# Kernel tuning notes

Measured on AMD Instinct MI355X. Metric: run time of the kernel, lower is better.

The kernel has to match this reference:

```python
import jax, jax.numpy as jnp
import numpy as np

N = 100000      # nodes
E = 1600000     # edges (avg degree 16)
F_IN = 64       # state_size
H = 128         # hidden_channels
L = 3           # nb_hidden_layers


def setup_inputs() -> dict:
    key = jax.random.key(0)
    ks = jax.random.split(key, 10)
    x = jax.random.normal(ks[0], (N, F_IN), dtype=jnp.float32)
    edge_index = jax.random.randint(ks[1], (2, E), 0, N, dtype=jnp.int32)
    # GCNConv params (glorot-ish scale), bias=True by default in PyG
    W1 = jax.random.normal(ks[2], (F_IN, H), jnp.float32) * (1.0 / np.sqrt(F_IN))
    b1 = jnp.zeros((H,), jnp.float32)
    W2 = jax.random.normal(ks[3], (L, H, H), jnp.float32) * (1.0 / np.sqrt(H))
    b2 = jnp.zeros((L, H), jnp.float32)
    W3 = jax.random.normal(ks[4], (H, 1), jnp.float32) * (1.0 / np.sqrt(H))
    b3 = jnp.zeros((1,), jnp.float32)
    return {"x": x, "edge_index": edge_index, "W1": W1, "b1": b1,
            "W2": W2, "b2": b2, "W3": W3, "b3": b3}


def _gcn_norm(edge_index):
    """Add self-loops and compute symmetric normalization (PyG GCNConv default)."""
    loop = jnp.arange(N, dtype=edge_index.dtype)
    src = jnp.concatenate([edge_index[0], loop])  # [E+N]
    dst = jnp.concatenate([edge_index[1], loop])
    deg = jax.ops.segment_sum(jnp.ones_like(dst, dtype=jnp.float32), dst, num_segments=N)
    dinv = jnp.where(deg > 0, jax.lax.rsqrt(deg), 0.0)
    norm = dinv[src] * dinv[dst]                  # [E+N]
    return src, dst, norm


def _gcn_conv(x, src, dst, norm, W, b):
    h = x @ W                                     # [N, F_out] linear first
    msg = h[src] * norm[:, None]                  # gather + scale, [E+N, F_out]
    agg = jax.ops.segment_sum(msg, dst, num_segments=N)  # scatter-add
    return agg + b


def reference(x, edge_index, W1, b1, W2, b2, W3, b3):
    src, dst, norm = _gcn_norm(edge_index)
    h = jax.nn.relu(_gcn_conv(x, src, dst, norm, W1, b1))
    for i in range(L):  # fixed small layer count
        h = jax.nn.relu(_gcn_conv(h, src, dst, norm, W2[i], b2[i]))
    out = _gcn_conv(h, src, dst, norm, W3, b3)    # [N, 1]
    return out
```

## Files before the change

kernel.cpp:

```cpp
#include <hip/hip_runtime.h>
#include <hip/hip_bf16.h>

#define DIV_UP(a,b) (((a)+(b)-1)/(b))

typedef __attribute__((ext_vector_type(8))) short short8v;
typedef __attribute__((ext_vector_type(4))) float f32x4;
typedef _Float16 half8v __attribute__((ext_vector_type(8)));

__device__ inline unsigned short f2bf(float f){
  unsigned u = __float_as_uint(f);
  u += 0x7FFFu + ((u >> 16) & 1u);
  return (unsigned short)(u >> 16);
}
__device__ inline float bf2f(unsigned short h){ return __uint_as_float(((unsigned)h) << 16); }

__global__ __launch_bounds__(256) void k_count_r(const int* __restrict__ dst, int* __restrict__ counts8,
                                                 int E, int N){
  const int g   = blockIdx.x & 7;
  const int bi  = blockIdx.x >> 3;
  const int bpg = gridDim.x >> 3;
  const int chunkE = (E + 7) >> 3;
  const int lo = g*chunkE;
  const int hi = min(lo + chunkE, E);
  int* base = counts8 + (size_t)g*N;
  for (int e = lo + bi*256 + threadIdx.x; e < hi; e += bpg*256)
    atomicAdd(&base[dst[e]], 1);
}

__global__ __launch_bounds__(256) void k_fill_g(const int* __restrict__ src, const int* __restrict__ dst,
                                                const int* __restrict__ rowptr, int* __restrict__ fill,
                                                int* __restrict__ csr, int E, int N){
  const int g   = blockIdx.x & 7;
  const int bi  = blockIdx.x >> 3;
  const int bpg = gridDim.x >> 3;
  const int chunk = (N + 7) >> 3;
  const int lo = g*chunk;
  const int hi = min(lo + chunk, N);
  for (int e = bi*256 + threadIdx.x; e < E; e += bpg*256){
    int d = dst[e];
    if (d >= lo && d < hi){
      int pos = rowptr[d] + atomicAdd(&fill[d], 1);
      csr[pos] = src[e];
    }
  }
}

__global__ __launch_bounds__(1024) void k_scan1(const int* __restrict__ counts8, int* __restrict__ rowptr,
                                                int* __restrict__ bsum, float* __restrict__ dinv, int N){
  __shared__ int s[1024];
  int t = threadIdx.x, g = blockIdx.x*1024 + t;
  int v = 0;
  if (g < N){
    #pragma unroll
    for (int j = 0; j < 8; ++j) v += counts8[(size_t)j*N + g];
    dinv[g] = rsqrtf((float)(v + 1));
  }
  s[t] = v; __syncthreads();
  for (int off = 1; off < 1024; off <<= 1){
    int u = (t >= off) ? s[t-off] : 0; __syncthreads();
    s[t] += u; __syncthreads();
  }
  if (g < N) rowptr[g] = s[t] - v;
  if (t == 1023) bsum[blockIdx.x] = s[1023];
}

__global__ __launch_bounds__(128) void k_scan2(const int* __restrict__ bsum, int* __restrict__ boff,
                                               int nb, int* __restrict__ rowptr, int N){
  __shared__ int s[128];
  int t = threadIdx.x;
  int v = (t < nb) ? bsum[t] : 0;
  s[t] = v; __syncthreads();
  for (int off = 1; off < 128; off <<= 1){
    int u = (t >= off) ? s[t-off] : 0; __syncthreads();
    s[t] += u; __syncthreads();
  }
  if (t < nb) boff[t] = s[t] - v;
  if (t == 127) rowptr[N] = s[127];
}

__global__ __launch_bounds__(1024) void k_scan3(int* __restrict__ rowptr, const int* __restrict__ boff, int N){
  int g = blockIdx.x*1024 + threadIdx.x;
  if (g < N) rowptr[g] += boff[blockIdx.x];
}

__global__ __launch_bounds__(256) void k_prep_x(const float* __restrict__ x, const float* __restrict__ dinv,
                                                _Float16* __restrict__ xs, int N){
  int idx = blockIdx.x*256 + threadIdx.x;
  if (idx >= N*8) return;
  int row = idx >> 3, c = (idx & 7) * 8;
  float d = dinv[row];
  float4 a = *(const float4*)(x + (size_t)row*64 + c);
  float4 b = *(const float4*)(x + (size_t)row*64 + c + 4);
  half8v o;
  o[0]=(_Float16)(d*a.x); o[1]=(_Float16)(d*a.y); o[2]=(_Float16)(d*a.z); o[3]=(_Float16)(d*a.w);
  o[4]=(_Float16)(d*b.x); o[5]=(_Float16)(d*b.y); o[6]=(_Float16)(d*b.z); o[7]=(_Float16)(d*b.w);
  *(half8v*)(xs + (size_t)row*64 + c) = o;
}

__global__ __launch_bounds__(256) void k_split_w(const float* __restrict__ W1, const float* __restrict__ W2,
                                                 unsigned short* __restrict__ W1h, unsigned short* __restrict__ W1l,
                                                 unsigned short* __restrict__ W2h, unsigned short* __restrict__ W2l,
                                                 int L){
  int idx = blockIdx.x*256 + threadIdx.x;
  int n1 = 64*128;
  if (idx < n1){
    int j = idx & 7, lane = (idx >> 3) & 63, t = idx >> 9;
    int kc = t >> 3, nt = t & 7;
    int tcol = lane & 15, quad = lane >> 4;
    int k = kc*32 + quad*8 + j, n = nt*16 + tcol;
    float v = W1[k*128 + n];
    unsigned short hi = f2bf(v);
    W1h[idx] = hi; W1l[idx] = f2bf(v - bf2f(hi));
  } else {
    int idx2 = idx - n1;
    if (idx2 >= L*128*128) return;
    int i = idx2 >> 14, r = idx2 & 16383;
    int j = r & 7, lane = (r >> 3) & 63, t = r >> 9;
    int kc = t >> 3, nt = t & 7;
    int tcol = lane & 15, quad = lane >> 4;
    int k = kc*32 + quad*8 + j, n = nt*16 + tcol;
    float v = W2[(size_t)i*16384 + k*128 + n];
    unsigned short hi = f2bf(v);
    W2h[idx2] = hi; W2l[idx2] = f2bf(v - bf2f(hi));
  }
}

__global__ __launch_bounds__(256) void k_layer1(const _Float16* __restrict__ xs, const int* __restrict__ rowptr,
                                                const int* __restrict__ csr, const float* __restrict__ dinv,
                                                const unsigned short* __restrict__ W1h, const unsigned short* __restrict__ W1l,
                                                const float* __restrict__ b1,
                                                const unsigned short* __restrict__ W2h0, const unsigned short* __restrict__ W2l0,
                                                _Float16* __restrict__ pout, int N){
  constexpr int XS = 72, HS = 136;
  __shared__ __align__(16) char smem[32*HS*2*2];
  unsigned short (*Xh)[XS] = (unsigned short(*)[XS])smem;
  unsigned short (*Xl)[XS] = (unsigned short(*)[XS])(smem + 32*XS*2);
  unsigned short (*Hh)[HS] = (unsigned short(*)[HS])smem;
  unsigned short (*Hl)[HS] = (unsigned short(*)[HS])(smem + 32*HS*2);

  const int tid = threadIdx.x;
  const int node0 = blockIdx.x*32;

  {
    const int nl = tid >> 3;
    const int c  = (tid & 7) * 8;
    const _Float16* xc = xs + c;
    int node = node0 + nl;
    if (node < N){
      const float dn = dinv[node];
      int e = rowptr[node], end = rowptr[node+1];
      half8v sv = *(const half8v*)(xs + (size_t)node*64 + c);
      float a[8];
      #pragma unroll
      for (int j = 0; j < 8; ++j) a[j] = (float)sv[j];
      for (; e + 4 <= end; e += 4){
        int s0 = csr[e], s1 = csr[e+1], s2 = csr[e+2], s3 = csr[e+3];
        half8v v0 = *(const half8v*)(xc + (size_t)s0*64);
        half8v v1 = *(const half8v*)(xc + (size_t)s1*64);
        half8v v2 = *(const half8v*)(xc + (size_t)s2*64);
        half8v v3 = *(const half8v*)(xc + (size_t)s3*64);
        #pragma unroll
        for (int j = 0; j < 8; ++j)
          a[j] += (float)v0[j] + (float)v1[j] + (float)v2[j] + (float)v3[j];
      }
      for (; e < end; ++e){
        half8v v = *(const half8v*)(xc + (size_t)csr[e]*64);
        #pragma unroll
        for (int j = 0; j < 8; ++j) a[j] += (float)v[j];
      }
      ushort4 hh0, hh1, hl0, hl1;
      unsigned short* hp0 = (unsigned short*)&hh0;
      unsigned short* hp1 = (unsigned short*)&hh1;
      unsigned short* lp0 = (unsigned short*)&hl0;
      unsigned short* lp1 = (unsigned short*)&hl1;
      #pragma unroll
      for (int j = 0; j < 8; ++j){
        float o = dn * a[j];
        unsigned short hi = f2bf(o);
        unsigned short lo = f2bf(o - bf2f(hi));
        if (j < 4){ hp0[j] = hi; lp0[j] = lo; } else { hp1[j-4] = hi; lp1[j-4] = lo; }
      }
      *(ushort4*)&Xh[nl][c]   = hh0;
      *(ushort4*)&Xh[nl][c+4] = hh1;
      *(ushort4*)&Xl[nl][c]   = hl0;
      *(ushort4*)&Xl[nl][c+4] = hl1;
    }
  }
  __syncthreads();

  const int wv = tid >> 6, lane = tid & 63, quad = lane >> 4, tcol = lane & 15;
  const int wrow = (wv >> 1) * 16;
  const int wcol = (wv & 1) * 64;

  f32x4 acc[4];
  #pragma unroll
  for (int t = 0; t < 4; ++t){ acc[t][0]=0.f; acc[t][1]=0.f; acc[t][2]=0.f; acc[t][3]=0.f; }
  #pragma unroll
  for (int kc = 0; kc < 2; ++kc){
    short8v a_h = *(const short8v*)&Xh[wrow + tcol][kc*32 + quad*8];
    short8v a_l = *(const short8v*)&Xl[wrow + tcol][kc*32 + quad*8];
    #pragma unroll
    for (int ntl = 0; ntl < 4; ++ntl){
      int nt = (wv & 1)*4 + ntl;
      short8v b_h = *(const short8v*)(W1h + ((size_t)(kc*8 + nt)*64 + lane)*8);
      short8v b_l = *(const short8v*)(W1l + ((size_t)(kc*8 + nt)*64 + lane)*8);
      acc[ntl] = __builtin_amdgcn_mfma_f32_16x16x32_bf16(a_h, b_h, acc[ntl], 0, 0, 0);
      acc[ntl] = __builtin_amdgcn_mfma_f32_16x16x32_bf16(a_l, b_h, acc[ntl], 0, 0, 0);
      acc[ntl] = __builtin_amdgcn_mfma_f32_16x16x32_bf16(a_h, b_l, acc[ntl], 0, 0, 0);
    }
  }
  __syncthreads();

  #pragma unroll
  for (int reg = 0; reg < 4; ++reg){
    int lrow = wrow + quad*4 + reg;
    #pragma unroll
    for (int ntl = 0; ntl < 4; ++ntl){
      int col = wcol + ntl*16 + tcol;
      float o = fmaxf(acc[ntl][reg] + b1[col], 0.f);
      unsigned short hi = f2bf(o);
      Hh[lrow][col] = hi;
      Hl[lrow][col] = f2bf(o - bf2f(hi));
    }
  }
  __syncthreads();

  #pragma unroll
  for (int t = 0; t < 4; ++t){ acc[t][0]=0.f; acc[t][1]=0.f; acc[t][2]=0.f; acc[t][3]=0.f; }
  #pragma unroll
  for (int kc = 0; kc < 4; ++kc){
    short8v a_h = *(const short8v*)&Hh[wrow + tcol][kc*32 + quad*8];
    short8v a_l = *(const short8v*)&Hl[wrow + tcol][kc*32 + quad*8];
    #pragma unroll
    for (int ntl = 0; ntl < 4; ++ntl){
      int nt = (wv & 1)*4 + ntl;
      short8v b_h = *(const short8v*)(W2h0 + ((size_t)(kc*8 + nt)*64 + lane)*8);
      short8v b_l = *(const short8v*)(W2l0 + ((size_t)(kc*8 + nt)*64 + lane)*8);
      acc[ntl] = __builtin_amdgcn_mfma_f32_16x16x32_bf16(a_h, b_h, acc[ntl], 0, 0, 0);
      acc[ntl] = __builtin_amdgcn_mfma_f32_16x16x32_bf16(a_l, b_h, acc[ntl], 0, 0, 0);
      acc[ntl] = __builtin_amdgcn_mfma_f32_16x16x32_bf16(a_h, b_l, acc[ntl], 0, 0, 0);
    }
  }
  #pragma unroll
  for (int reg = 0; reg < 4; ++reg){
    int grow = node0 + wrow + quad*4 + reg;
    if (grow < N){
      float sc = dinv[grow];
      _Float16* op = pout + (size_t)grow*128 + wcol + tcol;
      #pragma unroll
      for (int ntl = 0; ntl < 4; ++ntl) op[ntl*16] = (_Float16)(acc[ntl][reg] * sc);
    }
  }
}

__global__ __launch_bounds__(256) void k_fuse2(const _Float16* __restrict__ p, const int* __restrict__ rowptr,
                                               const int* __restrict__ csr, const float* __restrict__ dinv,
                                               const float* __restrict__ bias,
                                               const unsigned short* __restrict__ Bh, const unsigned short* __restrict__ Bl,
                                               _Float16* __restrict__ pout, int N){
  constexpr int HS = 136;
  __shared__ __align__(16) char smem[32*HS*2*2];
  unsigned short (*Hh)[HS] = (unsigned short(*)[HS])smem;
  unsigned short (*Hl)[HS] = (unsigned short(*)[HS])(smem + 32*HS*2);

  const int tid = threadIdx.x;
  const int node0 = blockIdx.x*32;

  {
    const int nl = tid >> 4;
    const int c  = (tid & 15) * 8;
    const _Float16* pc = p + c;
    #pragma unroll
    for (int it = 0; it < 2; ++it){
      int ln = it*16 + nl;
      int node = node0 + ln;
      if (node < N){
        int e = rowptr[node], end = rowptr[node+1];
        half8v sv = *(const half8v*)(p + (size_t)node*128 + c);
        float a[8];
        #pragma unroll
        for (int j = 0; j < 8; ++j) a[j] = (float)sv[j];
        for (; e + 4 <= end; e += 4){
          int s0 = csr[e], s1 = csr[e+1], s2 = csr[e+2], s3 = csr[e+3];
          half8v v0 = *(const half8v*)(pc + (size_t)s0*128);
          half8v v1 = *(const half8v*)(pc + (size_t)s1*128);
          half8v v2 = *(const half8v*)(pc + (size_t)s2*128);
          half8v v3 = *(const half8v*)(pc + (size_t)s3*128);
          #pragma unroll
          for (int j = 0; j < 8; ++j)
            a[j] += (float)v0[j] + (float)v1[j] + (float)v2[j] + (float)v3[j];
        }
        for (; e < end; ++e){
          half8v v = *(const half8v*)(pc + (size_t)csr[e]*128);
          #pragma unroll
          for (int j = 0; j < 8; ++j) a[j] += (float)v[j];
        }
        float d = dinv[node];
        short8v hh, hl;
        #pragma unroll
        for (int j = 0; j < 8; ++j){
          float o = fmaxf(d*a[j] + bias[c+j], 0.f);
          unsigned short hi = f2bf(o);
          hh[j] = (short)hi;
          hl[j] = (short)f2bf(o - bf2f(hi));
        }
        *(short8v*)&Hh[ln][c] = hh;
        *(short8v*)&Hl[ln][c] = hl;
      }
    }
  }
  __syncthreads();

  const int wv = tid >> 6, lane = tid & 63, quad = lane >> 4, tcol = lane & 15;
  const int wrow = (wv >> 1) * 16;
  const int wcol = (wv & 1) * 64;
  f32x4 acc[4];
  #pragma unroll
  for (int t = 0; t < 4; ++t){ acc[t][0]=0.f; acc[t][1]=0.f; acc[t][2]=0.f; acc[t][3]=0.f; }
  #pragma unroll
  for (int kc = 0; kc < 4; ++kc){
    short8v a_h = *(const short8v*)&Hh[wrow + tcol][kc*32 + quad*8];
    short8v a_l = *(const short8v*)&Hl[wrow + tcol][kc*32 + quad*8];
    #pragma unroll
    for (int ntl = 0; ntl < 4; ++ntl){
      int nt = (wv & 1)*4 + ntl;
      short8v b_h = *(const short8v*)(Bh + ((size_t)(kc*8 + nt)*64 + lane)*8);
      short8v b_l = *(const short8v*)(Bl + ((size_t)(kc*8 + nt)*64 + lane)*8);
      acc[ntl] = __builtin_amdgcn_mfma_f32_16x16x32_bf16(a_h, b_h, acc[ntl], 0, 0, 0);
      acc[ntl] = __builtin_amdgcn_mfma_f32_16x16x32_bf16(a_l, b_h, acc[ntl], 0, 0, 0);
      acc[ntl] = __builtin_amdgcn_mfma_f32_16x16x32_bf16(a_h, b_l, acc[ntl], 0, 0, 0);
    }
  }
  #pragma unroll
  for (int reg = 0; reg < 4; ++reg){
    int grow = node0 + wrow + quad*4 + reg;
    if (grow < N){
      float sc = dinv[grow];
      _Float16* op = pout + (size_t)grow*128 + wcol + tcol;
      #pragma unroll
      for (int ntl = 0; ntl < 4; ++ntl) op[ntl*16] = (_Float16)(acc[ntl][reg] * sc);
    }
  }
}

__global__ __launch_bounds__(256) void k_agg_last(const _Float16* __restrict__ p, const int* __restrict__ rowptr,
                                                  const int* __restrict__ csr, const float* __restrict__ dinv,
                                                  const float* __restrict__ bias, const float* __restrict__ W3,
                                                  float* __restrict__ p5, int N){
  const int tid = threadIdx.x;
  const int node = blockIdx.x*16 + (tid >> 4);
  if (node >= N) return;
  const int c = (tid & 15) * 8;
  const _Float16* pc = p + c;
  int e = rowptr[node], end = rowptr[node+1];
  half8v sv = *(const half8v*)(p + (size_t)node*128 + c);
  float a[8];
  #pragma unroll
  for (int j = 0; j < 8; ++j) a[j] = (float)sv[j];
  for (; e + 4 <= end; e += 4){
    int s0 = csr[e], s1 = csr[e+1], s2 = csr[e+2], s3 = csr[e+3];
    half8v v0 = *(const half8v*)(pc + (size_t)s0*128);
    half8v v1 = *(const half8v*)(pc + (size_t)s1*128);
    half8v v2 = *(const half8v*)(pc + (size_t)s2*128);
    half8v v3 = *(const half8v*)(pc + (size_t)s3*128);
    #pragma unroll
    for (int j = 0; j < 8; ++j)
      a[j] += (float)v0[j] + (float)v1[j] + (float)v2[j] + (float)v3[j];
  }
  for (; e < end; ++e){
    half8v v = *(const half8v*)(pc + (size_t)csr[e]*128);
    #pragma unroll
    for (int j = 0; j < 8; ++j) a[j] += (float)v[j];
  }
  float d = dinv[node];
  float sdot = 0.f;
  #pragma unroll
  for (int j = 0; j < 8; ++j){
    float o = fmaxf(d*a[j] + bias[c+j], 0.f);
    sdot += o * W3[c+j];
  }
  #pragma unroll
  for (int m = 8; m >= 1; m >>= 1) sdot += __shfl_xor(sdot, m, 16);
  if ((tid & 15) == 0) p5[node] = d * sdot;
}

__global__ __launch_bounds__(256) void k_agg1(const float* __restrict__ p5, const int* __restrict__ rowptr,
                                              const int* __restrict__ csr, const float* __restrict__ dinv,
                                              const float* __restrict__ b3, float* __restrict__ out, int N){
  int n = blockIdx.x*256 + threadIdx.x;
  if (n >= N) return;
  int e = rowptr[n], end = rowptr[n+1];
  float acc = p5[n];
  for (; e + 4 <= end; e += 4)
    acc += p5[csr[e]] + p5[csr[e+1]] + p5[csr[e+2]] + p5[csr[e+3]];
  for (; e < end; ++e) acc += p5[csr[e]];
  out[n] = dinv[n]*acc + b3[0];
}

extern "C" void kernel_launch(void* const* d_in, const int* in_sizes, int n_in,
                              void* d_out, int out_size, void* d_ws, size_t ws_size,
                              hipStream_t stream){
  const float* x  = (const float*)d_in[0];
  const int*   ei = (const int*)  d_in[1];
  const float* W1 = (const float*)d_in[2];
  const float* b1 = (const float*)d_in[3];
  const float* W2 = (const float*)d_in[4];
  const float* b2 = (const float*)d_in[5];
  const float* W3 = (const float*)d_in[6];
  const float* b3 = (const float*)d_in[7];
  float* out = (float*)d_out;

  const int N = in_sizes[0] / 64;
  const int E = in_sizes[1] / 2;
  const int L = in_sizes[4] / (128*128);
  const int* src = ei;
  const int* dst = ei + E;

  char* ws = (char*)d_ws;
  size_t off = 0;
  auto alloc = [&](size_t bytes){ void* p = ws + off; off += (bytes + 255) & ~(size_t)255; return p; };
  size_t c8b  = (((size_t)N*8*4) + 255) & ~(size_t)255;
  size_t cntb = ((size_t)N*4 + 255) & ~(size_t)255;
  int*   counts8 = (int*)alloc(c8b + cntb);
  int*   fillc   = (int*)((char*)counts8 + c8b);
  int*   rowptr = (int*)  alloc((size_t)(N+1)*4);
  int*   bsum   = (int*)  alloc(128*4);
  int*   boff   = (int*)  alloc(128*4);
  float* dinv   = (float*)alloc((size_t)N*4);
  float* p5     = (float*)alloc((size_t)N*4);
  int*   csr    = (int*)  alloc((size_t)E*4);
  _Float16* xs  = (_Float16*)alloc((size_t)N*64*2);
  _Float16* pA  = (_Float16*)alloc((size_t)N*128*2);
  _Float16* pB  = (_Float16*)alloc((size_t)N*128*2);
  unsigned short* W1h = (unsigned short*)alloc(64*128*2);
  unsigned short* W1l = (unsigned short*)alloc(64*128*2);
  unsigned short* W2h = (unsigned short*)alloc((size_t)L*128*128*2);
  unsigned short* W2l = (unsigned short*)alloc((size_t)L*128*128*2);
  (void)ws_size; (void)n_in; (void)out_size;

  hipMemsetAsync(counts8, 0, c8b + cntb, stream);

  k_count_r<<<1024,256,0,stream>>>(dst, counts8, E, N);
  int nb = DIV_UP(N,1024);
  k_scan1<<<nb,1024,0,stream>>>(counts8, rowptr, bsum, dinv, N);
  k_scan2<<<1,128,0,stream>>>(bsum, boff, nb, rowptr, N);
  k_scan3<<<nb,1024,0,stream>>>(rowptr, boff, N);
  k_fill_g<<<1024,256,0,stream>>>(src, dst, rowptr, fillc, csr, E, N);

  k_prep_x<<<DIV_UP(N*8,256),256,0,stream>>>(x, dinv, xs, N);

  int wtot = 64*128 + L*128*128;
  k_split_w<<<DIV_UP(wtot,256),256,0,stream>>>(W1, W2, W1h, W1l, W2h, W2l, L);

  k_layer1<<<DIV_UP(N,32),256,0,stream>>>(xs, rowptr, csr, dinv, W1h, W1l, b1, W2h, W2l, pA, N);
  _Float16* pin = pA; _Float16* pout = pB;
  for (int i = 1; i < L; ++i){
    k_fuse2<<<DIV_UP(N,32),256,0,stream>>>(pin, rowptr, csr, dinv, b2 + (size_t)(i-1)*128,
                                           W2h + (size_t)i*128*128, W2l + (size_t)i*128*128, pout, N);
    _Float16* t = pin; pin = pout; pout = t;
  }
  k_agg_last<<<DIV_UP(N,16),256,0,stream>>>(pin, rowptr, csr, dinv, b2 + (size_t)(L-1)*128, W3, p5, N);

  k_agg1<<<DIV_UP(N,256),256,0,stream>>>(p5, rowptr, csr, dinv, b3, out, N);
}
```

Before: 494.3 us.

## Split fused gather+GEMM into column-sliced gather kernel and dense kernel

The fused aggregate-then-GEMM kernels are split into a standalone gather kernel and a dense MFMA kernel. The gather kernel gives each block one 16-column slice of all nodes, so each sweep over the feature table touches a smaller working set that may fit in cache. Results go to a column-chunked intermediate buffer that the dense and last-layer kernels read. This adds an extra round trip of N×128 fp16 through memory, an extra launch per layer, and more scattered csr/rowptr reads, since every slice re-reads the index arrays.

```diff
diff --git a/kernel.cpp b/kernel.cpp
--- a/kernel.cpp
+++ b/kernel.cpp
@@ -253,8 +253,47 @@
   }
 }
 
-__global__ __launch_bounds__(256) void k_fuse2(const _Float16* __restrict__ p, const int* __restrict__ rowptr,
-                                               const int* __restrict__ csr, const float* __restrict__ dinv,
+__global__ __launch_bounds__(256) void k_gather_cs(const _Float16* __restrict__ p, const int* __restrict__ rowptr,
+                                                   const int* __restrict__ csr, _Float16* __restrict__ aggT, int N){
+  const int c    = blockIdx.x & 7;
+  const int node = (blockIdx.x >> 3)*256 + threadIdx.x;
+  if (node >= N) return;
+  const _Float16* pc = p + c*16;
+  float a[16];
+  {
+    half8v s0 = *(const half8v*)(pc + (size_t)node*128);
+    half8v s1 = *(const half8v*)(pc + (size_t)node*128 + 8);
+    #pragma unroll
+    for (int j = 0; j < 8; ++j){ a[j] = (float)s0[j]; a[8+j] = (float)s1[j]; }
+  }
+  int e = rowptr[node], end = rowptr[node+1];
+  for (; e + 2 <= end; e += 2){
+    int s0 = csr[e], s1 = csr[e+1];
+    half8v u0 = *(const half8v*)(pc + (size_t)s0*128);
+    half8v u1 = *(const half8v*)(pc + (size_t)s0*128 + 8);
+    half8v w0 = *(const half8v*)(pc + (size_t)s1*128);
+    half8v w1 = *(const half8v*)(pc + (size_t)s1*128 + 8);
+    #pragma unroll
+    for (int j = 0; j < 8; ++j){
+      a[j]   += (float)u0[j] + (float)w0[j];
+      a[8+j] += (float)u1[j] + (float)w1[j];
+    }
+  }
+  if (e < end){
+    int s0 = csr[e];
+    half8v u0 = *(const half8v*)(pc + (size_t)s0*128);
+    half8v u1 = *(const half8v*)(pc + (size_t)s0*128 + 8);
+    #pragma unroll
+    for (int j = 0; j < 8; ++j){ a[j] += (float)u0[j]; a[8+j] += (float)u1[j]; }
+  }
+  half8v o0, o1;
+  #pragma unroll
+  for (int j = 0; j < 8; ++j){ o0[j] = (_Float16)a[j]; o1[j] = (_Float16)a[8+j]; }
+  _Float16* dp = aggT + ((size_t)c*N + node)*16;
+  *(half8v*)dp = o0; *(half8v*)(dp + 8) = o1;
+}
+
+__global__ __launch_bounds__(256) void k_dense(const _Float16* __restrict__ aggT, const float* __restrict__ dinv,
                                                const float* __restrict__ bias,
                                                const unsigned short* __restrict__ Bh, const unsigned short* __restrict__ Bl,
                                                _Float16* __restrict__ pout, int N){
@@ -268,44 +307,25 @@
 
   {
     const int nl = tid >> 4;
-    const int c  = (tid & 15) * 8;
-    const _Float16* pc = p + c;
+    const int cB = (tid & 15) * 8;
+    const int ch = cB >> 4, co = cB & 15;
     #pragma unroll
     for (int it = 0; it < 2; ++it){
       int ln = it*16 + nl;
       int node = node0 + ln;
       if (node < N){
-        int e = rowptr[node], end = rowptr[node+1];
-        half8v sv = *(const half8v*)(p + (size_t)node*128 + c);
-        float a[8];
-        #pragma unroll
-        for (int j = 0; j < 8; ++j) a[j] = (float)sv[j];
-        for (; e + 4 <= end; e += 4){
-          int s0 = csr[e], s1 = csr[e+1], s2 = csr[e+2], s3 = csr[e+3];
-          half8v v0 = *(const half8v*)(pc + (size_t)s0*128);
-          half8v v1 = *(const half8v*)(pc + (size_t)s1*128);
-          half8v v2 = *(const half8v*)(pc + (size_t)s2*128);
-          half8v v3 = *(const half8v*)(pc + (size_t)s3*128);
-          #pragma unroll
-          for (int j = 0; j < 8; ++j)
-            a[j] += (float)v0[j] + (float)v1[j] + (float)v2[j] + (float)v3[j];
-        }
-        for (; e < end; ++e){
-          half8v v = *(const half8v*)(pc + (size_t)csr[e]*128);
-          #pragma unroll
-          for (int j = 0; j < 8; ++j) a[j] += (float)v[j];
-        }
+        half8v v = *(const half8v*)(aggT + ((size_t)ch*N + node)*16 + co);
         float d = dinv[node];
         short8v hh, hl;
         #pragma unroll
         for (int j = 0; j < 8; ++j){
-          float o = fmaxf(d*a[j] + bias[c+j], 0.f);
+          float o = fmaxf(d*(float)v[j] + bias[cB+j], 0.f);
           unsigned short hi = f2bf(o);
           hh[j] = (short)hi;
           hl[j] = (short)f2bf(o - bf2f(hi));
         }
-        *(short8v*)&Hh[ln][c] = hh;
-        *(short8v*)&Hl[ln][c] = hl;
+        *(short8v*)&Hh[ln][cB] = hh;
+        *(short8v*)&Hl[ln][cB] = hl;
       }
     }
   }
@@ -343,41 +363,21 @@
   }
 }
 
-__global__ __launch_bounds__(256) void k_agg_last(const _Float16* __restrict__ p, const int* __restrict__ rowptr,
-                                                  const int* __restrict__ csr, const float* __restrict__ dinv,
-                                                  const float* __restrict__ bias, const float* __restrict__ W3,
-                                                  float* __restrict__ p5, int N){
+__global__ __launch_bounds__(256) void k_dense_last(const _Float16* __restrict__ aggT, const float* __restrict__ dinv,
+                                                    const float* __restrict__ bias, const float* __restrict__ W3,
+                                                    float* __restrict__ p5, int N){
   const int tid = threadIdx.x;
   const int node = blockIdx.x*16 + (tid >> 4);
   if (node >= N) return;
-  const int c = (tid & 15) * 8;
-  const _Float16* pc = p + c;
-  int e = rowptr[node], end = rowptr[node+1];
-  half8v sv = *(const half8v*)(p + (size_t)node*128 + c);
-  float a[8];
-  #pragma unroll
-  for (int j = 0; j < 8; ++j) a[j] = (float)sv[j];
-  for (; e + 4 <= end; e += 4){
-    int s0 = csr[e], s1 = csr[e+1], s2 = csr[e+2], s3 = csr[e+3];
-    half8v v0 = *(const half8v*)(pc + (size_t)s0*128);
-    half8v v1 = *(const half8v*)(pc + (size_t)s1*128);
-    half8v v2 = *(const half8v*)(pc + (size_t)s2*128);
-    half8v v3 = *(const half8v*)(pc + (size_t)s3*128);
-    #pragma unroll
-    for (int j = 0; j < 8; ++j)
-      a[j] += (float)v0[j] + (float)v1[j] + (float)v2[j] + (float)v3[j];
-  }
-  for (; e < end; ++e){
-    half8v v = *(const half8v*)(pc + (size_t)csr[e]*128);
-    #pragma unroll
-    for (int j = 0; j < 8; ++j) a[j] += (float)v[j];
-  }
+  const int cB = (tid & 15) * 8;
+  const int ch = cB >> 4, co = cB & 15;
+  half8v v = *(const half8v*)(aggT + ((size_t)ch*N + node)*16 + co);
   float d = dinv[node];
   float sdot = 0.f;
   #pragma unroll
   for (int j = 0; j < 8; ++j){
-    float o = fmaxf(d*a[j] + bias[c+j], 0.f);
-    sdot += o * W3[c+j];
+    float o = fmaxf(d*(float)v[j] + bias[cB+j], 0.f);
+    sdot += o * W3[cB+j];
   }
   #pragma unroll
   for (int m = 8; m >= 1; m >>= 1) sdot += __shfl_xor(sdot, m, 16);
@@ -432,6 +432,7 @@
   _Float16* xs  = (_Float16*)alloc((size_t)N*64*2);
   _Float16* pA  = (_Float16*)alloc((size_t)N*128*2);
   _Float16* pB  = (_Float16*)alloc((size_t)N*128*2);
+  _Float16* aggT= (_Float16*)alloc((size_t)N*128*2);
   unsigned short* W1h = (unsigned short*)alloc(64*128*2);
   unsigned short* W1l = (unsigned short*)alloc(64*128*2);
   unsigned short* W2h = (unsigned short*)alloc((size_t)L*128*128*2);
@@ -454,12 +455,15 @@
 
   k_layer1<<<DIV_UP(N,32),256,0,stream>>>(xs, rowptr, csr, dinv, W1h, W1l, b1, W2h, W2l, pA, N);
   _Float16* pin = pA; _Float16* pout = pB;
+  const int gth = 8*DIV_UP(N,256);
   for (int i = 1; i < L; ++i){
-    k_fuse2<<<DIV_UP(N,32),256,0,stream>>>(pin, rowptr, csr, dinv, b2 + (size_t)(i-1)*128,
+    k_gather_cs<<<gth,256,0,stream>>>(pin, rowptr, csr, aggT, N);
+    k_dense<<<DIV_UP(N,32),256,0,stream>>>(aggT, dinv, b2 + (size_t)(i-1)*128,
                                            W2h + (size_t)i*128*128, W2l + (size_t)i*128*128, pout, N);
     _Float16* t = pin; pin = pout; pout = t;
   }
-  k_agg_last<<<DIV_UP(N,16),256,0,stream>>>(pin, rowptr, csr, dinv, b2 + (size_t)(L-1)*128, W3, p5, N);
+  k_gather_cs<<<gth,256,0,stream>>>(pin, rowptr, csr, aggT, N);
+  k_dense_last<<<DIV_UP(N,16),256,0,stream>>>(aggT, dinv, b2 + (size_t)(L-1)*128, W3, p5, N);
 
   k_agg1<<<DIV_UP(N,256),256,0,stream>>>(p5, rowptr, csr, dinv, b3, out, N);
 }
```

After: 1.092 ms. +121.0%, slower.

## Pre-bucket edges by destination range before CSR fill

Applied to the files above, without the earlier changes.

Adds a bucketing pass that partitions edges into 8 destination-range buckets, packing each (src, dst) pair into a 64-bit word. The CSR fill kernel then reads only its own bucket instead of every block scanning all E edges and discarding those outside its range, which cuts redundant dst reads by about 8x. The cost is an extra kernel, extra global writes and reads of packed edges, and a fixed per-bucket capacity (E/8 + 32768) that could overflow if the destinations are skewed.

```diff
diff --git a/kernel.cpp b/kernel.cpp
--- a/kernel.cpp
+++ b/kernel.cpp
@@ -27,21 +27,55 @@
     atomicAdd(&base[dst[e]], 1);
 }
 
-__global__ __launch_bounds__(256) void k_fill_g(const int* __restrict__ src, const int* __restrict__ dst,
-                                                const int* __restrict__ rowptr, int* __restrict__ fill,
-                                                int* __restrict__ csr, int E, int N){
+__global__ __launch_bounds__(256) void k_bucket(const int* __restrict__ src, const int* __restrict__ dst,
+                                                unsigned long long* __restrict__ bk, int* __restrict__ bcnt,
+                                                int E, int CH, int Ecap){
+  __shared__ int lcnt[8];
+  __shared__ int gbase[8];
+  const int base = blockIdx.x * 2048;
+  if (base >= E) return;
+  const int tid = threadIdx.x;
+  if (tid < 8) lcnt[tid] = 0;
+  __syncthreads();
+  int g[8], ls[8], sv[8], dv[8];
+  #pragma unroll
+  for (int j = 0; j < 8; ++j){
+    int e = base + j*256 + tid;
+    if (e < E){
+      sv[j] = src[e]; dv[j] = dst[e];
+      int gg = dv[j] / CH;
+      g[j] = gg;
+      ls[j] = atomicAdd(&lcnt[gg], 1);
+    }
+  }
+  __syncthreads();
+  if (tid < 8) gbase[tid] = atomicAdd(&bcnt[tid], lcnt[tid]);
+  __syncthreads();
+  #pragma unroll
+  for (int j = 0; j < 8; ++j){
+    int e = base + j*256 + tid;
+    if (e < E){
+      int gg = g[j];
+      bk[(size_t)gg*Ecap + gbase[gg] + ls[j]] =
+        ((unsigned long long)(unsigned)sv[j] << 32) | (unsigned)dv[j];
+    }
+  }
+}
+
+__global__ __launch_bounds__(256) void k_fill_b(const unsigned long long* __restrict__ bk, const int* __restrict__ bcnt,
+                                                const int* __restrict__ rowptr, int* __restrict__ fillc,
+                                                int* __restrict__ csr, int Ecap){
   const int g   = blockIdx.x & 7;
   const int bi  = blockIdx.x >> 3;
   const int bpg = gridDim.x >> 3;
-  const int chunk = (N + 7) >> 3;
-  const int lo = g*chunk;
-  const int hi = min(lo + chunk, N);
-  for (int e = bi*256 + threadIdx.x; e < E; e += bpg*256){
-    int d = dst[e];
-    if (d >= lo && d < hi){
-      int pos = rowptr[d] + atomicAdd(&fill[d], 1);
-      csr[pos] = src[e];
-    }
+  const int n   = bcnt[g];
+  const unsigned long long* b = bk + (size_t)g*Ecap;
+  for (int i = bi*256 + threadIdx.x; i < n; i += bpg*256){
+    unsigned long long pk = b[i];
+    int d = (int)(pk & 0xffffffffu);
+    int s = (int)(pk >> 32);
+    int pos = rowptr[d] + atomicAdd(&fillc[d], 1);
+    csr[pos] = s;
   }
 }
 
@@ -421,14 +455,19 @@
   auto alloc = [&](size_t bytes){ void* p = ws + off; off += (bytes + 255) & ~(size_t)255; return p; };
   size_t c8b  = (((size_t)N*8*4) + 255) & ~(size_t)255;
   size_t cntb = ((size_t)N*4 + 255) & ~(size_t)255;
-  int*   counts8 = (int*)alloc(c8b + cntb);
+  size_t bcb  = 256;
+  int*   counts8 = (int*)alloc(c8b + cntb + bcb);
   int*   fillc   = (int*)((char*)counts8 + c8b);
+  int*   bcnt    = (int*)((char*)counts8 + c8b + cntb);
   int*   rowptr = (int*)  alloc((size_t)(N+1)*4);
   int*   bsum   = (int*)  alloc(128*4);
   int*   boff   = (int*)  alloc(128*4);
   float* dinv   = (float*)alloc((size_t)N*4);
   float* p5     = (float*)alloc((size_t)N*4);
   int*   csr    = (int*)  alloc((size_t)E*4);
+  const int CH   = DIV_UP(N, 8);
+  const int Ecap = ((E + 7) >> 3) + 32768;
+  unsigned long long* bk = (unsigned long long*)alloc((size_t)8*Ecap*8);
   _Float16* xs  = (_Float16*)alloc((size_t)N*64*2);
   _Float16* pA  = (_Float16*)alloc((size_t)N*128*2);
   _Float16* pB  = (_Float16*)alloc((size_t)N*128*2);
@@ -438,14 +477,15 @@
   unsigned short* W2l = (unsigned short*)alloc((size_t)L*128*128*2);
   (void)ws_size; (void)n_in; (void)out_size;
 
-  hipMemsetAsync(counts8, 0, c8b + cntb, stream);
+  hipMemsetAsync(counts8, 0, c8b + cntb + bcb, stream);
 
   k_count_r<<<1024,256,0,stream>>>(dst, counts8, E, N);
+  k_bucket<<<DIV_UP(E,2048),256,0,stream>>>(src, dst, bk, bcnt, E, CH, Ecap);
   int nb = DIV_UP(N,1024);
   k_scan1<<<nb,1024,0,stream>>>(counts8, rowptr, bsum, dinv, N);
   k_scan2<<<1,128,0,stream>>>(bsum, boff, nb, rowptr, N);
   k_scan3<<<nb,1024,0,stream>>>(rowptr, boff, N);
-  k_fill_g<<<1024,256,0,stream>>>(src, dst, rowptr, fillc, csr, E, N);
+  k_fill_b<<<1024,256,0,stream>>>(bk, bcnt, rowptr, fillc, csr, Ecap);
 
   k_prep_x<<<DIV_UP(N*8,256),256,0,stream>>>(x, dinv, xs, N);
 
```

New measurement: 507.3 us. 2.6% more time.
